# Optimization experiments

Hardware: AMD Instinct MI355X
Metric: run time of the kernel (lower is better)

The kernel has to match this reference:

```python
import jax, jax.numpy as jnp
import numpy as np

EPS = 1e-12  # torch F.normalize eps

def setup_inputs() -> dict:
    key = jax.random.key(0)
    k1, k2, k3 = jax.random.split(key, 3)
    N, F_IN, F_OUT = 8192, 512, 256
    adjacency = jax.random.uniform(k1, (N, N), dtype=jnp.float32)
    input_feature = jax.random.normal(k2, (N, F_IN), dtype=jnp.float32)
    # xavier_normal_ with gain=1: std = sqrt(2/(fan_in+fan_out))
    std = float(np.sqrt(2.0 / (F_IN + F_OUT)))
    weight = jax.random.normal(k3, (F_IN, F_OUT), dtype=jnp.float32) * std
    bias = jnp.zeros((F_OUT,), dtype=jnp.float32)
    return {"adjacency": adjacency, "input_feature": input_feature,
            "weight": weight, "bias": bias}

def reference(adjacency, input_feature, weight, bias):
    # row L1 normalization, matching torch.nn.functional.normalize(p=1, dim=1)
    row_norm = jnp.sum(jnp.abs(adjacency), axis=1, keepdims=True)
    adj_n = adjacency / jnp.maximum(row_norm, EPS)
    support = adj_n @ input_feature            # [N, F_in]
    output = support @ weight + bias           # [N, F_out]
    return output
```

## Files before the change

kernel.cpp:

```cpp
#include <hip/hip_runtime.h>
#include <hip/hip_bf16.h>


typedef __attribute__((ext_vector_type(8))) __bf16 bf16x8;
typedef __attribute__((ext_vector_type(4))) float f32x4;

#define AS1 __attribute__((address_space(1)))
#define AS3 __attribute__((address_space(3)))

__device__ __forceinline__ void async_load16(const void* g, void* l) {
  __builtin_amdgcn_global_load_lds((const AS1 void*)g, (AS3 void*)l, 16, 0, 0);
}

__global__ __launch_bounds__(256) void transpose_cvt_kernel(
    const float* __restrict__ src, __hip_bfloat16* __restrict__ dst, int R, int C) {
  __shared__ float tile[64][65];
  const int t = threadIdx.x;
  const int nrb = R >> 6;
  const int rb = blockIdx.x % nrb, cb = blockIdx.x / nrb;
  const int r0 = rb * 64, c0 = cb * 64;
  const int lr = t >> 4, lc4 = (t & 15) * 4;
#pragma unroll
  for (int p = 0; p < 4; ++p) {
    const int r = p * 16 + lr;
    const f32x4 v = *(const f32x4*)(src + (size_t)(r0 + r) * C + c0 + lc4);
    tile[r][lc4 + 0] = v[0]; tile[r][lc4 + 1] = v[1];
    tile[r][lc4 + 2] = v[2]; tile[r][lc4 + 3] = v[3];
  }
  __syncthreads();
#pragma unroll
  for (int i = 0; i < 16; ++i) {
    const int idx = i * 256 + t;
    const int n = idx >> 6, k = idx & 63;
    dst[(size_t)(c0 + n) * R + r0 + k] = __float2bfloat16(tile[k][n]);
  }
}

__global__ __launch_bounds__(256) void gemm_xw_kernel(
    const float* __restrict__ X,
    const __hip_bfloat16* __restrict__ WT,
    float* __restrict__ Y)
{
  __shared__ char smem[49152];
  char* Sbase = smem;
  char* Wbase = smem + 16384;

  const int t = threadIdx.x;
  const int wave = t >> 6, lane = t & 63;
  const int quad = lane >> 4, l16 = lane & 15;

  const int b = blockIdx.x;
  const int xcd = b & 7, s = b >> 3;
  const int rb = xcd * 16 + (s >> 1), cb = s & 1;
  const int r0 = rb * 64, c0 = cb * 128;

  const int wm = wave & 1, wn = wave >> 1;

  f32x4 acc[2][4] = {};

  const int am = t >> 2;
  const int kq = t & 3;
  const float* sp = X + (size_t)(r0 + am) * 512 + kq * 16;
  const int sw0 = am * 128 + (((kq * 2 + 0) ^ (am & 7)) * 16);
  const int sw1 = am * 128 + (((kq * 2 + 1) ^ (am & 7)) * 16);

  f32x4 sreg[4];
#pragma unroll
  for (int i = 0; i < 4; ++i) sreg[i] = *(const f32x4*)(sp + i * 4);

#pragma unroll
  for (int i = 0; i < 4; ++i) {
    const int slot = i * 256 + t;
    const int n = slot >> 3;
    const int G = (slot & 7) ^ (n & 7);
    async_load16(WT + (size_t)(c0 + n) * 512 + G * 8, Wbase + slot * 16);
  }

  int cur = 0;
#pragma unroll 2
  for (int kt = 0; kt < 8; ++kt) {
    {
      char* sw = Sbase + cur * 8192;
      bf16x8 v0, v1;
#pragma unroll
      for (int j = 0; j < 4; ++j) {
        v0[j]     = (__bf16)(sreg[0][j]);
        v0[j + 4] = (__bf16)(sreg[1][j]);
        v1[j]     = (__bf16)(sreg[2][j]);
        v1[j + 4] = (__bf16)(sreg[3][j]);
      }
      *(bf16x8*)(sw + sw0) = v0;
      *(bf16x8*)(sw + sw1) = v1;
    }
    __syncthreads();

    if (kt < 7) {
      const float* spk = sp + (kt + 1) * 64;
#pragma unroll
      for (int i = 0; i < 4; ++i) sreg[i] = *(const f32x4*)(spk + i * 4);
#pragma unroll
      for (int i = 0; i < 4; ++i) {
        const int slot = i * 256 + t;
        const int n = slot >> 3;
        const int G = (slot & 7) ^ (n & 7);
        async_load16(WT + (size_t)(c0 + n) * 512 + (kt + 1) * 64 + G * 8,
                     Wbase + (cur ^ 1) * 16384 + slot * 16);
      }
    }

    {
      const char* sb = Sbase + cur * 8192;
      const char* wb = Wbase + cur * 16384;
      bf16x8 af[2][2];
#pragma unroll
      for (int rt = 0; rt < 2; ++rt) {
        const int row = wm * 32 + rt * 16 + l16;
#pragma unroll
        for (int kb = 0; kb < 2; ++kb) {
          const int ch = (kb * 4 + quad) ^ (row & 7);
          af[rt][kb] = *(const bf16x8*)(sb + row * 128 + ch * 16);
        }
      }
#pragma unroll
      for (int ct = 0; ct < 4; ++ct) {
        const int n = wn * 64 + ct * 16 + l16;
#pragma unroll
        for (int kb = 0; kb < 2; ++kb) {
          const int ch = (kb * 4 + quad) ^ (n & 7);
          const bf16x8 bfr = *(const bf16x8*)(wb + n * 128 + ch * 16);
#pragma unroll
          for (int rt = 0; rt < 2; ++rt)
            acc[rt][ct] = __builtin_amdgcn_mfma_f32_16x16x32_bf16(
                af[rt][kb], bfr, acc[rt][ct], 0, 0, 0);
        }
      }
    }
    cur ^= 1;
  }

#pragma unroll
  for (int rt = 0; rt < 2; ++rt) {
#pragma unroll
    for (int r = 0; r < 4; ++r) {
      const int row_l = wm * 32 + rt * 16 + quad * 4 + r;
#pragma unroll
      for (int ct = 0; ct < 4; ++ct) {
        const int col_l = wn * 64 + ct * 16 + l16;
        Y[(size_t)(r0 + row_l) * 256 + c0 + col_l] = acc[rt][ct][r];
      }
    }
  }
}

__global__ __launch_bounds__(1024, 4) void gemm_ay_kernel(
    const float* __restrict__ A,
    const __hip_bfloat16* __restrict__ YT,
    float* __restrict__ Pb,
    float* __restrict__ Rb,
    int atomic_flag)
{
  __shared__ char smem[65536];
  char* Abase = smem;
  char* Ybase = smem + 32768;
  float* rsmem = (float*)Ybase;

  const int t = threadIdx.x;
  const int wave = t >> 6, lane = t & 63;
  const int quad = lane >> 4, l16 = lane & 15;

  const int b = blockIdx.x;
  const int ks = b & 7;
  const int rb = b >> 3;
  const int r0 = rb * 256;
  const int k0 = ks * 1024;

  const int wm = wave & 3, wn = wave >> 2;

  f32x4 acc[4][4] = {};
  float rs = 0.0f;

  const int am = t >> 2;
  const int kc = t & 3;
  const float* ap = A + (size_t)(r0 + am) * 8192 + k0 + kc * 8;
  const int aw_off = (am >> 1) * 128 + (((kc + 4 * (am & 1)) ^ ((am >> 1) & 7)) * 16);

  f32x4 areg[2];
  areg[0] = *(const f32x4*)(ap);
  areg[1] = *(const f32x4*)(ap + 4);

  {
    const int q = t >> 3;
    const int u = (t & 7) ^ (q & 7);
    const int n = 2 * q + (u >> 2), g = u & 3;
    async_load16(YT + (size_t)n * 8192 + k0 + g * 8, Ybase + t * 16);
  }

  int cur = 0;
#pragma unroll 2
  for (int kt = 0; kt < 32; ++kt) {
    {
      const f32x4 e = areg[0], o = areg[1];
      rs += fabsf(e[0]) + fabsf(e[1]) + fabsf(e[2]) + fabsf(e[3]) +
            fabsf(o[0]) + fabsf(o[1]) + fabsf(o[2]) + fabsf(o[3]);
      bf16x8 v;
      v[0] = (__bf16)e[0]; v[1] = (__bf16)e[1]; v[2] = (__bf16)e[2]; v[3] = (__bf16)e[3];
      v[4] = (__bf16)o[0]; v[5] = (__bf16)o[1]; v[6] = (__bf16)o[2]; v[7] = (__bf16)o[3];
      *(bf16x8*)(Abase + cur * 16384 + aw_off) = v;
    }
    __syncthreads();

    if (kt < 31) {
      const float* apk = ap + (kt + 1) * 32;
      areg[0] = *(const f32x4*)(apk);
      areg[1] = *(const f32x4*)(apk + 4);
      const int q = t >> 3;
      const int u = (t & 7) ^ (q & 7);
      const int n = 2 * q + (u >> 2), g = u & 3;
      async_load16(YT + (size_t)n * 8192 + k0 + (kt + 1) * 32 + g * 8,
                   Ybase + (cur ^ 1) * 16384 + t * 16);
    }

    {
      const char* ab = Abase + cur * 16384;
      const char* xb = Ybase + cur * 16384;
      bf16x8 af[4];
#pragma unroll
      for (int rt = 0; rt < 4; ++rt) {
        const int row = wm * 64 + rt * 16 + l16;
        const int off = (row >> 1) * 128 + (((quad + 4 * (row & 1)) ^ ((row >> 1) & 7)) * 16);
        af[rt] = *(const bf16x8*)(ab + off);
      }
#pragma unroll
      for (int ct = 0; ct < 4; ++ct) {
        const int n = wn * 64 + ct * 16 + l16;
        const int off = (n >> 1) * 128 + (((quad + 4 * (n & 1)) ^ ((n >> 1) & 7)) * 16);
        const bf16x8 bfr = *(const bf16x8*)(xb + off);
#pragma unroll
        for (int rt = 0; rt < 4; ++rt)
          acc[rt][ct] = __builtin_amdgcn_mfma_f32_16x16x32_bf16(
              af[rt], bfr, acc[rt][ct], 0, 0, 0);
      }
    }
    cur ^= 1;
  }

  rsmem[t] = rs;
  __syncthreads();
  if (t < 256) {
    const float v = rsmem[4 * t] + rsmem[4 * t + 1] + rsmem[4 * t + 2] + rsmem[4 * t + 3];
    if (atomic_flag) atomicAdd(&Rb[r0 + t], v);
    else             Rb[(size_t)ks * 8192 + r0 + t] = v;
  }

  if (atomic_flag) {
#pragma unroll
    for (int rt = 0; rt < 4; ++rt)
#pragma unroll
      for (int r = 0; r < 4; ++r) {
        const int row_l = wm * 64 + rt * 16 + quad * 4 + r;
#pragma unroll
        for (int ct = 0; ct < 4; ++ct) {
          const int col_l = wn * 64 + ct * 16 + l16;
          atomicAdd(&Pb[(size_t)(r0 + row_l) * 256 + col_l], acc[rt][ct][r]);
        }
      }
  } else {
    float* dst = Pb + (size_t)ks * (8192 * 256);
#pragma unroll
    for (int rt = 0; rt < 4; ++rt)
#pragma unroll
      for (int r = 0; r < 4; ++r) {
        const int row_l = wm * 64 + rt * 16 + quad * 4 + r;
#pragma unroll
        for (int ct = 0; ct < 4; ++ct) {
          const int col_l = wn * 64 + ct * 16 + l16;
          dst[(size_t)(r0 + row_l) * 256 + col_l] = acc[rt][ct][r];
        }
      }
  }
}

__global__ __launch_bounds__(256) void finalize_kernel(
    const float* __restrict__ Pb,
    const float* __restrict__ Rb,
    const float* __restrict__ bias,
    float* __restrict__ Out,
    int S)
{
  const int idx = blockIdx.x * 256 + threadIdx.x;
  const int i  = idx >> 6;
  const int j4 = (idx & 63) << 2;
  float rsum = 0.0f;
  for (int s = 0; s < S; ++s) rsum += Rb[(size_t)s * 8192 + i];
  const float inv = 1.0f / fmaxf(rsum, 1e-12f);
  f32x4 a = {};
  for (int s = 0; s < S; ++s) {
    const f32x4 p = *(const f32x4*)(Pb + (size_t)s * (8192 * 256) + (size_t)i * 256 + j4);
    a += p;
  }
  const f32x4 bv = *(const f32x4*)(bias + j4);
  const f32x4 o = a * inv + bv;
  *(f32x4*)(Out + (size_t)i * 256 + j4) = o;
}

extern "C" void kernel_launch(void* const* d_in, const int* in_sizes, int n_in,
                              void* d_out, int out_size, void* d_ws, size_t ws_size,
                              hipStream_t stream) {
  const float* A    = (const float*)d_in[0];
  const float* Xf   = (const float*)d_in[1];
  const float* Wf   = (const float*)d_in[2];
  const float* bias = (const float*)d_in[3];
  float* Out = (float*)d_out;

  char* ws = (char*)d_ws;
  __hip_bfloat16* WT = (__hip_bfloat16*)ws;
  __hip_bfloat16* YT = (__hip_bfloat16*)(ws + 262144);
  float*          Y  = (float*)(ws + 4456448);
  char*         tail = ws + 12845056;

  const size_t need_plain = 12845056ull + 67108864ull + 262144ull;
  float* Pb; float* Rb; int atomic_flag; int S;
  if (ws_size >= need_plain) {
    Pb = (float*)tail;
    Rb = (float*)(tail + 67108864);
    atomic_flag = 0; S = 8;
  } else {
    Pb = (float*)tail;
    Rb = (float*)(tail + 8388608);
    atomic_flag = 1; S = 1;
    hipMemsetAsync(tail, 0, 8388608 + 32768, stream);
  }

  transpose_cvt_kernel<<<32, 256, 0, stream>>>(Wf, WT, 512, 256);
  gemm_xw_kernel<<<256, 256, 0, stream>>>(Xf, WT, Y);
  transpose_cvt_kernel<<<512, 256, 0, stream>>>(Y, YT, 8192, 256);
  gemm_ay_kernel<<<256, 1024, 0, stream>>>(A, YT, Pb, Rb, atomic_flag);
  finalize_kernel<<<2048, 256, 0, stream>>>(Pb, Rb, bias, Out, S);
}
```

Measured before the change: 440.3 us.

## Fuse Y transpose into XW GEMM epilogue and shrink AY GEMM tiles

The XW GEMM now transposes its accumulator tile through shared memory and writes bf16 YT directly. This removes the separate fp32 Y buffer and the extra transpose-convert kernel launch. Separately, the A·Y GEMM block is halved to 512 threads covering 128 rows, with twice as many blocks and less shared memory. That should allow more concurrent blocks per CU, at the cost of each Y tile being loaded by more blocks.

```diff
diff --git a/kernel.cpp b/kernel.cpp
--- a/kernel.cpp
+++ b/kernel.cpp
@@ -39,7 +39,7 @@
 __global__ __launch_bounds__(256) void gemm_xw_kernel(
     const float* __restrict__ X,
     const __hip_bfloat16* __restrict__ WT,
-    float* __restrict__ Y)
+    __hip_bfloat16* __restrict__ YT)
 {
   __shared__ char smem[49152];
   char* Sbase = smem;
@@ -138,6 +138,8 @@
     cur ^= 1;
   }
 
+  __syncthreads();
+  __hip_bfloat16* Tr = (__hip_bfloat16*)smem;
 #pragma unroll
   for (int rt = 0; rt < 2; ++rt) {
 #pragma unroll
@@ -146,22 +148,30 @@
 #pragma unroll
       for (int ct = 0; ct < 4; ++ct) {
         const int col_l = wn * 64 + ct * 16 + l16;
-        Y[(size_t)(r0 + row_l) * 256 + c0 + col_l] = acc[rt][ct][r];
-      }
-    }
-  }
-}
-
-__global__ __launch_bounds__(1024, 4) void gemm_ay_kernel(
+        Tr[col_l * 64 + row_l] = __float2bfloat16(acc[rt][ct][r]);
+      }
+    }
+  }
+  __syncthreads();
+#pragma unroll
+  for (int i = 0; i < 4; ++i) {
+    const int c = i * 256 + t;
+    const int col = c >> 3, part = c & 7;
+    *(f32x4*)(YT + (size_t)(c0 + col) * 8192 + r0 + part * 8) =
+        *(const f32x4*)(Tr + col * 64 + part * 8);
+  }
+}
+
+__global__ __launch_bounds__(512, 4) void gemm_ay_kernel(
     const float* __restrict__ A,
     const __hip_bfloat16* __restrict__ YT,
     float* __restrict__ Pb,
     float* __restrict__ Rb,
     int atomic_flag)
 {
-  __shared__ char smem[65536];
+  __shared__ char smem[49152];
   char* Abase = smem;
-  char* Ybase = smem + 32768;
+  char* Ybase = smem + 16384;
   float* rsmem = (float*)Ybase;
 
   const int t = threadIdx.x;
@@ -171,10 +181,10 @@
   const int b = blockIdx.x;
   const int ks = b & 7;
   const int rb = b >> 3;
-  const int r0 = rb * 256;
+  const int r0 = rb * 128;
   const int k0 = ks * 1024;
 
-  const int wm = wave & 3, wn = wave >> 2;
+  const int wm = wave & 1, wn = wave >> 1;
 
   f32x4 acc[4][4] = {};
   float rs = 0.0f;
@@ -188,11 +198,13 @@
   areg[0] = *(const f32x4*)(ap);
   areg[1] = *(const f32x4*)(ap + 4);
 
-  {
-    const int q = t >> 3;
-    const int u = (t & 7) ^ (q & 7);
+#pragma unroll
+  for (int i = 0; i < 2; ++i) {
+    const int s = i * 512 + t;
+    const int q = s >> 3;
+    const int u = (s & 7) ^ (q & 7);
     const int n = 2 * q + (u >> 2), g = u & 3;
-    async_load16(YT + (size_t)n * 8192 + k0 + g * 8, Ybase + t * 16);
+    async_load16(YT + (size_t)n * 8192 + k0 + g * 8, Ybase + s * 16);
   }
 
   int cur = 0;
@@ -205,7 +217,7 @@
       bf16x8 v;
       v[0] = (__bf16)e[0]; v[1] = (__bf16)e[1]; v[2] = (__bf16)e[2]; v[3] = (__bf16)e[3];
       v[4] = (__bf16)o[0]; v[5] = (__bf16)o[1]; v[6] = (__bf16)o[2]; v[7] = (__bf16)o[3];
-      *(bf16x8*)(Abase + cur * 16384 + aw_off) = v;
+      *(bf16x8*)(Abase + cur * 8192 + aw_off) = v;
     }
     __syncthreads();
 
@@ -213,15 +225,19 @@
       const float* apk = ap + (kt + 1) * 32;
       areg[0] = *(const f32x4*)(apk);
       areg[1] = *(const f32x4*)(apk + 4);
-      const int q = t >> 3;
-      const int u = (t & 7) ^ (q & 7);
-      const int n = 2 * q + (u >> 2), g = u & 3;
-      async_load16(YT + (size_t)n * 8192 + k0 + (kt + 1) * 32 + g * 8,
-                   Ybase + (cur ^ 1) * 16384 + t * 16);
+#pragma unroll
+      for (int i = 0; i < 2; ++i) {
+        const int s = i * 512 + t;
+        const int q = s >> 3;
+        const int u = (s & 7) ^ (q & 7);
+        const int n = 2 * q + (u >> 2), g = u & 3;
+        async_load16(YT + (size_t)n * 8192 + k0 + (kt + 1) * 32 + g * 8,
+                     Ybase + (cur ^ 1) * 16384 + s * 16);
+      }
     }
 
     {
-      const char* ab = Abase + cur * 16384;
+      const char* ab = Abase + cur * 8192;
       const char* xb = Ybase + cur * 16384;
       bf16x8 af[4];
 #pragma unroll
@@ -246,7 +262,7 @@
 
   rsmem[t] = rs;
   __syncthreads();
-  if (t < 256) {
+  if (t < 128) {
     const float v = rsmem[4 * t] + rsmem[4 * t + 1] + rsmem[4 * t + 2] + rsmem[4 * t + 3];
     if (atomic_flag) atomicAdd(&Rb[r0 + t], v);
     else             Rb[(size_t)ks * 8192 + r0 + t] = v;
@@ -315,10 +331,9 @@
   char* ws = (char*)d_ws;
   __hip_bfloat16* WT = (__hip_bfloat16*)ws;
   __hip_bfloat16* YT = (__hip_bfloat16*)(ws + 262144);
-  float*          Y  = (float*)(ws + 4456448);
-  char*         tail = ws + 12845056;
-
-  const size_t need_plain = 12845056ull + 67108864ull + 262144ull;
+  char*         tail = ws + 4456448;
+
+  const size_t need_plain = 4456448ull + 67108864ull + 262144ull;
   float* Pb; float* Rb; int atomic_flag; int S;
   if (ws_size >= need_plain) {
     Pb = (float*)tail;
@@ -332,8 +347,7 @@
   }
 
   transpose_cvt_kernel<<<32, 256, 0, stream>>>(Wf, WT, 512, 256);
-  gemm_xw_kernel<<<256, 256, 0, stream>>>(Xf, WT, Y);
-  transpose_cvt_kernel<<<512, 256, 0, stream>>>(Y, YT, 8192, 256);
-  gemm_ay_kernel<<<256, 1024, 0, stream>>>(A, YT, Pb, Rb, atomic_flag);
+  gemm_xw_kernel<<<256, 256, 0, stream>>>(Xf, WT, YT);
+  gemm_ay_kernel<<<512, 512, 0, stream>>>(A, YT, Pb, Rb, atomic_flag);
   finalize_kernel<<<2048, 256, 0, stream>>>(Pb, Rb, bias, Out, S);
 }
```

New measurement: 435.1 us. No clear change (-1.2%).
